# Kernel tuning notes

Hardware: AMD Instinct MI355X
Metric: run time of the kernel (lower is better)

The kernel has to match this reference:

```python
import jax, jax.numpy as jnp
import numpy as np

B, N, D, D_OUT = 8, 2048, 256, 256
LN_EPS = 1e-5
LRELU_SLOPE = 0.01


def setup_inputs() -> dict:
    key = jax.random.key(0)
    ks = jax.random.split(key, 11)
    s_in = 1.0 / np.sqrt(D)
    s_out = 1.0 / np.sqrt(D)
    return {
        "x_local": jax.random.normal(ks[0], (B, N, D), dtype=jnp.float32),
        "Wq": jax.random.uniform(ks[1], (D, D), jnp.float32, -s_in, s_in),
        "bq": jax.random.uniform(ks[2], (D,), jnp.float32, -s_in, s_in),
        "Wk": jax.random.uniform(ks[3], (D, D), jnp.float32, -s_in, s_in),
        "bk": jax.random.uniform(ks[4], (D,), jnp.float32, -s_in, s_in),
        "Wv": jax.random.uniform(ks[5], (D, D), jnp.float32, -s_in, s_in),
        "bv": jax.random.uniform(ks[6], (D,), jnp.float32, -s_in, s_in),
        "Wo": jax.random.uniform(ks[7], (D_OUT, D), jnp.float32, -s_out, s_out),
        "bo": jax.random.uniform(ks[8], (D_OUT,), jnp.float32, -s_out, s_out),
        "ln_gamma": jnp.ones((D_OUT,), jnp.float32),
        "ln_beta": jnp.zeros((D_OUT,), jnp.float32),
    }


def reference(x_local, Wq, bq, Wk, bk, Wv, bv, Wo, bo, ln_gamma, ln_beta):
    # Linear layers (torch convention: y = x @ W.T + b)
    Q = jnp.einsum("bnd,ed->bne", x_local, Wq) + bq
    K = jnp.einsum("bnd,ed->bne", x_local, Wk) + bk
    V = jnp.einsum("bnd,ed->bne", x_local, Wv) + bv
    # Unscaled attention (source applies no 1/sqrt(d))
    scores = jnp.einsum("bnd,bmd->bnm", Q, K)          # [B, N, N]
    attn = jax.nn.softmax(scores, axis=-1)
    loc = jnp.einsum("bnm,bmd->bnd", attn, V)           # [B, N, D]
    # fc_out: Linear -> LayerNorm -> LeakyReLU
    h = jnp.einsum("bnd,ed->bne", loc, Wo) + bo          # [B, N, D_OUT]
    mu = jnp.mean(h, axis=-1, keepdims=True)
    var = jnp.mean(jnp.square(h - mu), axis=-1, keepdims=True)
    hn = (h - mu) / jnp.sqrt(var + LN_EPS) * ln_gamma + ln_beta
    return jnp.where(hn >= 0, hn, LRELU_SLOPE * hn)
```

## Files before the change

### kernel.cpp

```cpp
#include <hip/hip_runtime.h>

typedef unsigned short u16;
typedef __attribute__((ext_vector_type(8))) _Float16 f16x8;
typedef __attribute__((ext_vector_type(4))) float f32x4;

#define MFMA_F16 __builtin_amdgcn_mfma_f32_16x16x32_f16

static __device__ __forceinline__ u16 f2h(float f) {
    return __builtin_bit_cast(u16, (_Float16)f);
}
static __device__ __forceinline__ ushort4 f4_to_h4(const float4 v) {
    ushort4 r;
    r.x = f2h(v.x); r.y = f2h(v.y); r.z = f2h(v.z); r.w = f2h(v.w);
    return r;
}

__global__ __launch_bounds__(256) void prep_w(
    const float* __restrict__ wq, const float* __restrict__ wk,
    const float* __restrict__ wv, const float* __restrict__ wo,
    u16* __restrict__ w4)
{
    const int tid = blockIdx.x * 256 + threadIdx.x;
    for (int i = tid; i < 65536; i += 16384) {
        const float* src = (i < 16384) ? wq : (i < 32768) ? wk
                         : (i < 49152) ? wv : wo;
        ((ushort4*)w4)[i] = f4_to_h4(((const float4*)src)[i & 16383]);
    }
}

__global__ __launch_bounds__(256) void proj_qkv(
    const float* __restrict__ X, const u16* __restrict__ w4,
    const float* __restrict__ bq, const float* __restrict__ bk,
    const float* __restrict__ bv,
    u16* __restrict__ Qh, u16* __restrict__ Kh, u16* __restrict__ Vt)
{
    const int z = blockIdx.y;
    const u16* __restrict__ W     = w4 + z * 65536;
    const float* __restrict__ bias = (z == 0) ? bq : (z == 1) ? bk : bv;

    const int m0   = blockIdx.x * 64;
    const int t    = threadIdx.x;
    const int w    = t >> 6;
    const int lane = t & 63;
    const int quad = lane >> 4;
    const int l16  = lane & 15;

    __shared__ __align__(16) u16 smem[18432];
    u16* Xs = smem;
    u16* Ws = smem + 2560;

    f32x4 acc[16];
#pragma unroll
    for (int i = 0; i < 16; ++i) acc[i] = f32x4{0.f, 0.f, 0.f, 0.f};

    for (int kc = 0; kc < 8; ++kc) {
#pragma unroll
        for (int i = 0; i < 2; ++i) {
            const int ch = i * 256 + t;
            const int row = ch >> 3, cg = ch & 7;
            const float4 v = *(const float4*)&X[(size_t)(m0 + row) * 256 + kc * 32 + cg * 4];
            *(ushort4*)&Xs[row * 40 + cg * 4] = f4_to_h4(v);
        }
#pragma unroll
        for (int i = 0; i < 4; ++i) {
            const int ch = i * 256 + t;
            const int row = ch >> 2, cg = ch & 3;
            *(int4*)&Ws[row * 40 + cg * 8] =
                *(const int4*)&W[(size_t)row * 256 + kc * 32 + cg * 8];
        }
        __syncthreads();

        const f16x8 af = *(const f16x8*)&Xs[(w * 16 + l16) * 40 + quad * 8];
#pragma unroll
        for (int nt = 0; nt < 16; ++nt) {
            const f16x8 bf = *(const f16x8*)&Ws[(nt * 16 + l16) * 40 + quad * 8];
            acc[nt] = MFMA_F16(af, bf, acc[nt], 0, 0, 0);
        }
        __syncthreads();
    }

    if (z < 2) {
        u16* __restrict__ Y = (z == 0) ? Qh : Kh;
#pragma unroll
        for (int nt = 0; nt < 16; ++nt) {
            const int col = nt * 16 + l16;
            const float bb = bias[col];
#pragma unroll
            for (int r = 0; r < 4; ++r)
                smem[(w * 16 + quad * 4 + r) * 264 + col] = f2h(acc[nt][r] + bb);
        }
        __syncthreads();
#pragma unroll
        for (int i = 0; i < 8; ++i) {
            const int ch = i * 256 + t;
            const int row = ch >> 5, cg = ch & 31;
            *(int4*)&Y[(size_t)(m0 + row) * 256 + cg * 8] =
                *(const int4*)&smem[row * 264 + cg * 8];
        }
    } else {
        const int b  = m0 >> 11;
        const int n0 = m0 & 2047;
#pragma unroll
        for (int nt = 0; nt < 16; ++nt) {
            const int col = nt * 16 + l16;
            const float bb = bias[col];
            ushort4 h4;
            h4.x = f2h(acc[nt][0] + bb);
            h4.y = f2h(acc[nt][1] + bb);
            h4.z = f2h(acc[nt][2] + bb);
            h4.w = f2h(acc[nt][3] + bb);
            *(ushort4*)&smem[col * 72 + w * 16 + quad * 4] = h4;
        }
        __syncthreads();
#pragma unroll
        for (int i = 0; i < 8; ++i) {
            const int ch = i * 256 + t;
            const int row = ch >> 3, cg = ch & 7;
            *(int4*)&Vt[(size_t)b * 524288 + (size_t)row * 2048 + n0 + cg * 8] =
                *(const int4*)&smem[row * 72 + cg * 8];
        }
    }
}

__global__ __launch_bounds__(256) void attn(
    const u16* __restrict__ Qh, const u16* __restrict__ Kg,
    const u16* __restrict__ Vt, u16* __restrict__ Op,
    u16* __restrict__ OutS, float* __restrict__ lmpL, float* __restrict__ lmpM)
{
    const int nz = gridDim.z;
    const int z  = blockIdx.z;
    const int tbase = 64 / nz, trem = 64 % nz;
    const int my_tiles = tbase + (z < trem ? 1 : 0);
    const int tile0    = tbase * z + (z < trem ? z : trem);

    const int b  = blockIdx.y;
    const int q0 = blockIdx.x * 64;
    const int t    = threadIdx.x;
    const int w    = t >> 6;
    const int lane = t & 63;
    const int quad = lane >> 4;
    const int l16  = lane & 15;

    __shared__ __align__(16) u16 smem[18688];
    u16* Ks = smem;
    u16* Vs = smem + 8448;
    u16* Os = smem;

    f16x8 qf[8];
    {
        const size_t qrow = (size_t)(b * 2048 + q0 + w * 16 + l16) * 256;
#pragma unroll
        for (int kc = 0; kc < 8; ++kc)
            qf[kc] = *(const f16x8*)&Qh[qrow + kc * 32 + quad * 8];
    }

    f32x4 O[16];
#pragma unroll
    for (int i = 0; i < 16; ++i) O[i] = f32x4{0.f, 0.f, 0.f, 0.f};
    float mrow = -1e30f, lrow = 0.f;

    for (int it = 0; it < my_tiles; ++it) {
        const int kt = (tile0 + it) * 32;
#pragma unroll
        for (int i = 0; i < 4; ++i) {
            const int ch = i * 256 + t;
            const int row = ch >> 5, cg = ch & 31;
            const int prow = ((row >> 2) & 3) * 8 + (row >> 4) * 4 + (row & 3);
            *(int4*)&Ks[row * 264 + cg * 8] =
                *(const int4*)&Kg[(size_t)(b * 2048 + kt + prow) * 256 + cg * 8];
        }
#pragma unroll
        for (int i = 0; i < 4; ++i) {
            const int ch = i * 256 + t;
            const int row = ch >> 2, cg = ch & 3;
            *(int4*)&Vs[row * 40 + cg * 8] =
                *(const int4*)&Vt[(size_t)b * 524288 + (size_t)row * 2048 + kt + cg * 8];
        }
        __syncthreads();

        f32x4 S[2];
        S[0] = f32x4{0.f, 0.f, 0.f, 0.f};
        S[1] = f32x4{0.f, 0.f, 0.f, 0.f};
        __builtin_amdgcn_s_setprio(1);
#pragma unroll
        for (int kc = 0; kc < 8; ++kc) {
#pragma unroll
            for (int kn = 0; kn < 2; ++kn) {
                const f16x8 kf = *(const f16x8*)&Ks[(kn * 16 + l16) * 264 + kc * 32 + quad * 8];
                S[kn] = MFMA_F16(kf, qf[kc], S[kn], 0, 0, 0);
            }
        }
        __builtin_amdgcn_s_setprio(0);

        float mt = fmaxf(fmaxf(fmaxf(S[0][0], S[0][1]), fmaxf(S[0][2], S[0][3])),
                         fmaxf(fmaxf(S[1][0], S[1][1]), fmaxf(S[1][2], S[1][3])));
        mt = fmaxf(mt, __shfl_xor(mt, 16));
        mt = fmaxf(mt, __shfl_xor(mt, 32));
        if (__any(mt - mrow > 8.f)) {
            const float mnew = fmaxf(mrow, mt);
            const float a = __expf(mrow - mnew);
            lrow *= a;
#pragma unroll
            for (int dv = 0; dv < 16; ++dv)
#pragma unroll
                for (int r = 0; r < 4; ++r) O[dv][r] *= a;
            mrow = mnew;
        }
        float p[2][4];
        float s = 0.f;
#pragma unroll
        for (int kn = 0; kn < 2; ++kn)
#pragma unroll
            for (int r = 0; r < 4; ++r) {
                p[kn][r] = __expf(S[kn][r] - mrow);
                s += p[kn][r];
            }
        s += __shfl_xor(s, 16);
        s += __shfl_xor(s, 32);
        lrow += s;

        f16x8 pf;
#pragma unroll
        for (int kn = 0; kn < 2; ++kn)
#pragma unroll
            for (int r = 0; r < 4; ++r)
                pf[kn * 4 + r] = (_Float16)p[kn][r];

        __builtin_amdgcn_s_setprio(1);
#pragma unroll
        for (int dvt = 0; dvt < 16; ++dvt) {
            const f16x8 vf = *(const f16x8*)&Vs[(dvt * 16 + l16) * 40 + quad * 8];
            O[dvt] = MFMA_F16(vf, pf, O[dvt], 0, 0, 0);
        }
        __builtin_amdgcn_s_setprio(0);
        __syncthreads();
    }

    {
        const float rl = 1.0f / lrow;
#pragma unroll
        for (int dvt = 0; dvt < 16; ++dvt) {
            ushort4 h4;
            h4.x = f2h(O[dvt][0] * rl);
            h4.y = f2h(O[dvt][1] * rl);
            h4.z = f2h(O[dvt][2] * rl);
            h4.w = f2h(O[dvt][3] * rl);
            *(ushort4*)&Os[(w * 16 + l16) * 264 + dvt * 16 + quad * 4] = h4;
        }
        if (quad == 0) {
            const int grow = b * 2048 + q0 + w * 16 + l16;
            lmpL[z * 16384 + grow] = lrow;
            lmpM[z * 16384 + grow] = mrow;
        }
    }
    __syncthreads();

    {
        const int row = t >> 2;
        if (z < 2) {
            u16* __restrict__ Oz = Op + (size_t)z * 4194304;
#pragma unroll
            for (int i = 0; i < 8; ++i) {
                const int chunk = (t & 3) * 8 + i;
                *(int4*)&Oz[(size_t)(b * 2048 + q0 + row) * 256 + chunk * 8] =
                    *(const int4*)&Os[row * 264 + chunk * 8];
            }
        } else {
            u16* __restrict__ Oz = OutS + (size_t)(z - 2) * 256;
#pragma unroll
            for (int i = 0; i < 8; ++i) {
                const int chunk = (t & 3) * 8 + i;
                *(int4*)&Oz[(size_t)(b * 2048 + q0 + row) * 512 + chunk * 8] =
                    *(const int4*)&Os[row * 264 + chunk * 8];
            }
        }
    }
}

__global__ __launch_bounds__(256) void outproj_ln(
    const u16* __restrict__ Op, const u16* __restrict__ OutS,
    const float* __restrict__ lmpL, const float* __restrict__ lmpM,
    const u16* __restrict__ Woh, const float* __restrict__ bo,
    const float* __restrict__ gamma, const float* __restrict__ beta,
    float* __restrict__ out)
{
    const int m0   = blockIdx.x * 64;
    const int t    = threadIdx.x;
    const int w    = t >> 6;
    const int lane = t & 63;
    const int quad = lane >> 4;
    const int l16  = lane & 15;

    __shared__ __align__(16) u16 Ls[64 * 40];
    __shared__ __align__(16) u16 Ws[256 * 40];
    __shared__ _Float16 wls[4][64];

    if (t < 64) {
        const float l0 = lmpL[m0 + t],         l1 = lmpL[16384 + m0 + t];
        const float l2 = lmpL[32768 + m0 + t], l3 = lmpL[49152 + m0 + t];
        const float m0v = lmpM[m0 + t],          m1v = lmpM[16384 + m0 + t];
        const float m2v = lmpM[32768 + m0 + t],  m3v = lmpM[49152 + m0 + t];
        const float mm = fmaxf(fmaxf(m0v, m1v), fmaxf(m2v, m3v));
        const float u0 = l0 * __expf(m0v - mm);
        const float u1 = l1 * __expf(m1v - mm);
        const float u2 = l2 * __expf(m2v - mm);
        const float u3 = l3 * __expf(m3v - mm);
        const float inv = 1.0f / (u0 + u1 + u2 + u3);
        wls[0][t] = (_Float16)(u0 * inv);
        wls[1][t] = (_Float16)(u1 * inv);
        wls[2][t] = (_Float16)(u2 * inv);
        wls[3][t] = (_Float16)(u3 * inv);
    }
    __syncthreads();

    f32x4 acc[16];
#pragma unroll
    for (int i = 0; i < 16; ++i) acc[i] = f32x4{0.f, 0.f, 0.f, 0.f};

    for (int kc = 0; kc < 8; ++kc) {
        {
            const int row = t >> 2, cg = t & 3;
            const size_t off  = (size_t)(m0 + row) * 256 + kc * 32 + cg * 8;
            const size_t offS = (size_t)(m0 + row) * 512 + kc * 32 + cg * 8;
            const f16x8 o0 = __builtin_bit_cast(f16x8, *(const int4*)&Op[off]);
            const f16x8 o1 = __builtin_bit_cast(f16x8, *(const int4*)&Op[4194304 + off]);
            const f16x8 o2 = __builtin_bit_cast(f16x8, *(const int4*)&OutS[offS]);
            const f16x8 o3 = __builtin_bit_cast(f16x8, *(const int4*)&OutS[offS + 256]);
            const _Float16 w0 = wls[0][row], w1 = wls[1][row];
            const _Float16 w2 = wls[2][row], w3 = wls[3][row];
            f16x8 lw;
#pragma unroll
            for (int j = 0; j < 8; ++j)
                lw[j] = o0[j] * w0 + o1[j] * w1 + o2[j] * w2 + o3[j] * w3;
            *(int4*)&Ls[row * 40 + cg * 8] = __builtin_bit_cast(int4, lw);
        }
#pragma unroll
        for (int i = 0; i < 4; ++i) {
            const int ch = i * 256 + t;
            const int row = ch >> 2, cg = ch & 3;
            *(int4*)&Ws[row * 40 + cg * 8] =
                *(const int4*)&Woh[(size_t)row * 256 + kc * 32 + cg * 8];
        }
        __syncthreads();

        const f16x8 af = *(const f16x8*)&Ls[(w * 16 + l16) * 40 + quad * 8];
#pragma unroll
        for (int nt = 0; nt < 16; ++nt) {
            const f16x8 bf = *(const f16x8*)&Ws[(nt * 16 + l16) * 40 + quad * 8];
            acc[nt] = MFMA_F16(af, bf, acc[nt], 0, 0, 0);
        }
        __syncthreads();
    }

    float g[16], bt[16], bb[16];
#pragma unroll
    for (int nt = 0; nt < 16; ++nt) {
        const int col = nt * 16 + l16;
        bb[nt] = bo[col]; g[nt] = gamma[col]; bt[nt] = beta[col];
    }

#pragma unroll
    for (int r = 0; r < 4; ++r) {
        float h[16];
        float sh = 0.f, sh2 = 0.f;
#pragma unroll
        for (int nt = 0; nt < 16; ++nt) {
            h[nt] = acc[nt][r] + bb[nt];
            sh  += h[nt];
            sh2 += h[nt] * h[nt];
        }
        sh  += __shfl_xor(sh, 1);  sh  += __shfl_xor(sh, 2);
        sh  += __shfl_xor(sh, 4);  sh  += __shfl_xor(sh, 8);
        sh2 += __shfl_xor(sh2, 1); sh2 += __shfl_xor(sh2, 2);
        sh2 += __shfl_xor(sh2, 4); sh2 += __shfl_xor(sh2, 8);
        const float mu  = sh * (1.f / 256.f);
        const float var = fmaxf(sh2 * (1.f / 256.f) - mu * mu, 0.f);
        const float rs  = rsqrtf(var + 1e-5f);
        const size_t row = (size_t)(m0 + w * 16 + quad * 4 + r) * 256;
#pragma unroll
        for (int nt = 0; nt < 16; ++nt) {
            const float hn = (h[nt] - mu) * rs * g[nt] + bt[nt];
            out[row + nt * 16 + l16] = (hn >= 0.f) ? hn : 0.01f * hn;
        }
    }
}

extern "C" void kernel_launch(void* const* d_in, const int* in_sizes, int n_in,
                              void* d_out, int out_size, void* d_ws, size_t ws_size,
                              hipStream_t stream)
{
    const float* x  = (const float*)d_in[0];
    const float* Wq = (const float*)d_in[1];
    const float* bq = (const float*)d_in[2];
    const float* Wk = (const float*)d_in[3];
    const float* bk = (const float*)d_in[4];
    const float* Wv = (const float*)d_in[5];
    const float* bv = (const float*)d_in[6];
    const float* Wo = (const float*)d_in[7];
    const float* bo = (const float*)d_in[8];
    const float* gm = (const float*)d_in[9];
    const float* bt = (const float*)d_in[10];
    float* out = (float*)d_out;

    u16* W4 = (u16*)d_ws;
    u16* Qh = W4 + 262144;
    u16* Kh = Qh + 4194304;
    u16* Vt = Kh + 4194304;
    u16* Op = Vt + 4194304;
    float* lmpM = (float*)(Op + 2 * 4194304);
    float* lmpL = (float*)W4;
    u16* Woh = W4 + 196608;
    u16* OutS = (u16*)d_out;

    prep_w     <<<64,             256, 0, stream>>>(Wq, Wk, Wv, Wo, W4);
    proj_qkv   <<<dim3(256, 3),   256, 0, stream>>>(x, W4, bq, bk, bv, Qh, Kh, Vt);
    attn       <<<dim3(32, 8, 4), 256, 0, stream>>>(Qh, Kh, Vt, Op, OutS, lmpL, lmpM);
    outproj_ln <<<256,            256, 0, stream>>>(Op, OutS, lmpL, lmpM, Woh, bo, gm, bt, out);
}
```

Before: 194.2 us.

## Prefetch next K-chunk into registers across projection, attention and out-proj kernels

```diff
diff --git a/kernel.cpp b/kernel.cpp
--- a/kernel.cpp
+++ b/kernel.cpp
@@ -53,28 +53,75 @@
 #pragma unroll
     for (int i = 0; i < 16; ++i) acc[i] = f32x4{0.f, 0.f, 0.f, 0.f};
 
+    float4 xst[2];
+    int4   wst[4];
+#pragma unroll
+    for (int i = 0; i < 2; ++i) {
+        const int ch = i * 256 + t;
+        const int row = ch >> 3, cg = ch & 7;
+        xst[i] = *(const float4*)&X[(size_t)(m0 + row) * 256 + cg * 4];
+    }
+#pragma unroll
+    for (int i = 0; i < 4; ++i) {
+        const int ch = i * 256 + t;
+        const int row = ch >> 2, cg = ch & 3;
+        wst[i] = *(const int4*)&W[(size_t)row * 256 + cg * 8];
+    }
+#pragma unroll
+    for (int i = 0; i < 2; ++i) {
+        const int ch = i * 256 + t;
+        const int row = ch >> 3, cg = ch & 7;
+        *(ushort4*)&Xs[row * 40 + cg * 4] = f4_to_h4(xst[i]);
+    }
+#pragma unroll
+    for (int i = 0; i < 4; ++i) {
+        const int ch = i * 256 + t;
+        const int row = ch >> 2, cg = ch & 3;
+        *(int4*)&Ws[row * 40 + cg * 8] = wst[i];
+    }
+    __syncthreads();
+
     for (int kc = 0; kc < 8; ++kc) {
-#pragma unroll
-        for (int i = 0; i < 2; ++i) {
-            const int ch = i * 256 + t;
-            const int row = ch >> 3, cg = ch & 7;
-            const float4 v = *(const float4*)&X[(size_t)(m0 + row) * 256 + kc * 32 + cg * 4];
-            *(ushort4*)&Xs[row * 40 + cg * 4] = f4_to_h4(v);
-        }
-#pragma unroll
-        for (int i = 0; i < 4; ++i) {
-            const int ch = i * 256 + t;
-            const int row = ch >> 2, cg = ch & 3;
-            *(int4*)&Ws[row * 40 + cg * 8] =
-                *(const int4*)&W[(size_t)row * 256 + kc * 32 + cg * 8];
-        }
-        __syncthreads();
+        const bool hasnext = (kc < 7);
+        if (hasnext) {
+            const int kn = kc + 1;
+#pragma unroll
+            for (int i = 0; i < 2; ++i) {
+                const int ch = i * 256 + t;
+                const int row = ch >> 3, cg = ch & 7;
+                xst[i] = *(const float4*)&X[(size_t)(m0 + row) * 256 + kn * 32 + cg * 4];
+            }
+#pragma unroll
+            for (int i = 0; i < 4; ++i) {
+                const int ch = i * 256 + t;
+                const int row = ch >> 2, cg = ch & 3;
+                wst[i] = *(const int4*)&W[(size_t)row * 256 + kn * 32 + cg * 8];
+            }
+        }
 
         const f16x8 af = *(const f16x8*)&Xs[(w * 16 + l16) * 40 + quad * 8];
+        __builtin_amdgcn_s_setprio(1);
 #pragma unroll
         for (int nt = 0; nt < 16; ++nt) {
             const f16x8 bf = *(const f16x8*)&Ws[(nt * 16 + l16) * 40 + quad * 8];
             acc[nt] = MFMA_F16(af, bf, acc[nt], 0, 0, 0);
+        }
+        __builtin_amdgcn_s_setprio(0);
+        __syncthreads();
+
+        if (hasnext) {
+#pragma unroll
+            for (int i = 0; i < 2; ++i) {
+                const int ch = i * 256 + t;
+                const int row = ch >> 3, cg = ch & 7;
+                *(ushort4*)&Xs[row * 40 + cg * 4] = f4_to_h4(xst[i]);
+            }
+#pragma unroll
+            for (int i = 0; i < 4; ++i) {
+                const int ch = i * 256 + t;
+                const int row = ch >> 2, cg = ch & 3;
+                *(int4*)&Ws[row * 40 + cg * 8] = wst[i];
+            }
         }
         __syncthreads();
     }
@@ -122,7 +169,7 @@
     }
 }
 
-__global__ __launch_bounds__(256) void attn(
+__global__ __launch_bounds__(256, 2) void attn(
     const u16* __restrict__ Qh, const u16* __restrict__ Kg,
     const u16* __restrict__ Vt, u16* __restrict__ Op,
     u16* __restrict__ OutS, float* __restrict__ lmpL, float* __restrict__ lmpM)
@@ -141,9 +188,7 @@
     const int quad = lane >> 4;
     const int l16  = lane & 15;
 
-    __shared__ __align__(16) u16 smem[18688];
-    u16* Ks = smem;
-    u16* Vs = smem + 8448;
+    __shared__ __align__(16) u16 smem[2 * 18688];
     u16* Os = smem;
 
     f16x8 qf[8];
@@ -159,24 +204,59 @@
     for (int i = 0; i < 16; ++i) O[i] = f32x4{0.f, 0.f, 0.f, 0.f};
     float mrow = -1e30f, lrow = 0.f;
 
-    for (int it = 0; it < my_tiles; ++it) {
-        const int kt = (tile0 + it) * 32;
+    int4 kst[4], vst[4];
+    {
+        const int kt = tile0 * 32;
 #pragma unroll
         for (int i = 0; i < 4; ++i) {
             const int ch = i * 256 + t;
             const int row = ch >> 5, cg = ch & 31;
             const int prow = ((row >> 2) & 3) * 8 + (row >> 4) * 4 + (row & 3);
-            *(int4*)&Ks[row * 264 + cg * 8] =
-                *(const int4*)&Kg[(size_t)(b * 2048 + kt + prow) * 256 + cg * 8];
+            kst[i] = *(const int4*)&Kg[(size_t)(b * 2048 + kt + prow) * 256 + cg * 8];
         }
 #pragma unroll
         for (int i = 0; i < 4; ++i) {
             const int ch = i * 256 + t;
             const int row = ch >> 2, cg = ch & 3;
-            *(int4*)&Vs[row * 40 + cg * 8] =
-                *(const int4*)&Vt[(size_t)b * 524288 + (size_t)row * 2048 + kt + cg * 8];
-        }
-        __syncthreads();
+            vst[i] = *(const int4*)&Vt[(size_t)b * 524288 + (size_t)row * 2048 + kt + cg * 8];
+        }
+#pragma unroll
+        for (int i = 0; i < 4; ++i) {
+            const int ch = i * 256 + t;
+            const int row = ch >> 5, cg = ch & 31;
+            *(int4*)&smem[row * 264 + cg * 8] = kst[i];
+        }
+#pragma unroll
+        for (int i = 0; i < 4; ++i) {
+            const int ch = i * 256 + t;
+            const int row = ch >> 2, cg = ch & 3;
+            *(int4*)&smem[8448 + row * 40 + cg * 8] = vst[i];
+        }
+    }
+    __syncthreads();
+
+    for (int it = 0; it < my_tiles; ++it) {
+        u16* __restrict__ Kc = smem + (it & 1) * 18688;
+        u16* __restrict__ Vc = Kc + 8448;
+        u16* __restrict__ Kn = smem + ((it & 1) ^ 1) * 18688;
+        u16* __restrict__ Vn = Kn + 8448;
+        const bool hasnext = (it + 1 < my_tiles);
+        if (hasnext) {
+            const int kt = (tile0 + it + 1) * 32;
+#pragma unroll
+            for (int i = 0; i < 4; ++i) {
+                const int ch = i * 256 + t;
+                const int row = ch >> 5, cg = ch & 31;
+                const int prow = ((row >> 2) & 3) * 8 + (row >> 4) * 4 + (row & 3);
+                kst[i] = *(const int4*)&Kg[(size_t)(b * 2048 + kt + prow) * 256 + cg * 8];
+            }
+#pragma unroll
+            for (int i = 0; i < 4; ++i) {
+                const int ch = i * 256 + t;
+                const int row = ch >> 2, cg = ch & 3;
+                vst[i] = *(const int4*)&Vt[(size_t)b * 524288 + (size_t)row * 2048 + kt + cg * 8];
+            }
+        }
 
         f32x4 S[2];
         S[0] = f32x4{0.f, 0.f, 0.f, 0.f};
@@ -186,7 +266,7 @@
         for (int kc = 0; kc < 8; ++kc) {
 #pragma unroll
             for (int kn = 0; kn < 2; ++kn) {
-                const f16x8 kf = *(const f16x8*)&Ks[(kn * 16 + l16) * 264 + kc * 32 + quad * 8];
+                const f16x8 kf = *(const f16x8*)&Kc[(kn * 16 + l16) * 264 + kc * 32 + quad * 8];
                 S[kn] = MFMA_F16(kf, qf[kc], S[kn], 0, 0, 0);
             }
         }
@@ -219,20 +299,35 @@
         s += __shfl_xor(s, 32);
         lrow += s;
 
-        f16x8 pf;
+        f16x8 pfv;
 #pragma unroll
         for (int kn = 0; kn < 2; ++kn)
 #pragma unroll
             for (int r = 0; r < 4; ++r)
-                pf[kn * 4 + r] = (_Float16)p[kn][r];
+                pfv[kn * 4 + r] = (_Float16)p[kn][r];
 
         __builtin_amdgcn_s_setprio(1);
 #pragma unroll
         for (int dvt = 0; dvt < 16; ++dvt) {
-            const f16x8 vf = *(const f16x8*)&Vs[(dvt * 16 + l16) * 40 + quad * 8];
-            O[dvt] = MFMA_F16(vf, pf, O[dvt], 0, 0, 0);
+            const f16x8 vf = *(const f16x8*)&Vc[(dvt * 16 + l16) * 40 + quad * 8];
+            O[dvt] = MFMA_F16(vf, pfv, O[dvt], 0, 0, 0);
         }
         __builtin_amdgcn_s_setprio(0);
+
+        if (hasnext) {
+#pragma unroll
+            for (int i = 0; i < 4; ++i) {
+                const int ch = i * 256 + t;
+                const int row = ch >> 5, cg = ch & 31;
+                *(int4*)&Kn[row * 264 + cg * 8] = kst[i];
+            }
+#pragma unroll
+            for (int i = 0; i < 4; ++i) {
+                const int ch = i * 256 + t;
+                const int row = ch >> 2, cg = ch & 3;
+                *(int4*)&Vn[row * 40 + cg * 8] = vst[i];
+            }
+        }
         __syncthreads();
     }
 
@@ -294,6 +389,24 @@
     __shared__ __align__(16) u16 Ls[64 * 40];
     __shared__ __align__(16) u16 Ws[256 * 40];
     __shared__ _Float16 wls[4][64];
+
+    const int orow = t >> 2, ocg = t & 3;
+
+    int4 ost[4], wst[4];
+    {
+        const size_t off  = (size_t)(m0 + orow) * 256 + ocg * 8;
+        const size_t offS = (size_t)(m0 + orow) * 512 + ocg * 8;
+        ost[0] = *(const int4*)&Op[off];
+        ost[1] = *(const int4*)&Op[4194304 + off];
+        ost[2] = *(const int4*)&OutS[offS];
+        ost[3] = *(const int4*)&OutS[offS + 256];
+    }
+#pragma unroll
+    for (int i = 0; i < 4; ++i) {
+        const int ch = i * 256 + t;
+        const int row = ch >> 2, cg = ch & 3;
+        wst[i] = *(const int4*)&Woh[(size_t)row * 256 + cg * 8];
+    }
 
     if (t < 64) {
         const float l0 = lmpL[m0 + t],         l1 = lmpL[16384 + m0 + t];
@@ -313,41 +426,77 @@
     }
     __syncthreads();
 
+    {
+        const _Float16 w0 = wls[0][orow], w1 = wls[1][orow];
+        const _Float16 w2 = wls[2][orow], w3 = wls[3][orow];
+        const f16x8 o0 = __builtin_bit_cast(f16x8, ost[0]);
+        const f16x8 o1 = __builtin_bit_cast(f16x8, ost[1]);
+        const f16x8 o2 = __builtin_bit_cast(f16x8, ost[2]);
+        const f16x8 o3 = __builtin_bit_cast(f16x8, ost[3]);
+        f16x8 lw;
+#pragma unroll
+        for (int j = 0; j < 8; ++j)
+            lw[j] = o0[j] * w0 + o1[j] * w1 + o2[j] * w2 + o3[j] * w3;
+        *(int4*)&Ls[orow * 40 + ocg * 8] = __builtin_bit_cast(int4, lw);
+    }
+#pragma unroll
+    for (int i = 0; i < 4; ++i) {
+        const int ch = i * 256 + t;
+        const int row = ch >> 2, cg = ch & 3;
+        *(int4*)&Ws[row * 40 + cg * 8] = wst[i];
+    }
+    __syncthreads();
+
     f32x4 acc[16];
 #pragma unroll
     for (int i = 0; i < 16; ++i) acc[i] = f32x4{0.f, 0.f, 0.f, 0.f};
 
     for (int kc = 0; kc < 8; ++kc) {
-        {
-            const int row = t >> 2, cg = t & 3;
-            const size_t off  = (size_t)(m0 + row) * 256 + kc * 32 + cg * 8;
-            const size_t offS = (size_t)(m0 + row) * 512 + kc * 32 + cg * 8;
-            const f16x8 o0 = __builtin_bit_cast(f16x8, *(const int4*)&Op[off]);
-            const f16x8 o1 = __builtin_bit_cast(f16x8, *(const int4*)&Op[4194304 + off]);
-            const f16x8 o2 = __builtin_bit_cast(f16x8, *(const int4*)&OutS[offS]);
-            const f16x8 o3 = __builtin_bit_cast(f16x8, *(const int4*)&OutS[offS + 256]);
-            const _Float16 w0 = wls[0][row], w1 = wls[1][row];
-            const _Float16 w2 = wls[2][row], w3 = wls[3][row];
-            f16x8 lw;
-#pragma unroll
-            for (int j = 0; j < 8; ++j)
-                lw[j] = o0[j] * w0 + o1[j] * w1 + o2[j] * w2 + o3[j] * w3;
-            *(int4*)&Ls[row * 40 + cg * 8] = __builtin_bit_cast(int4, lw);
-        }
-#pragma unroll
-        for (int i = 0; i < 4; ++i) {
-            const int ch = i * 256 + t;
-            const int row = ch >> 2, cg = ch & 3;
-            *(int4*)&Ws[row * 40 + cg * 8] =
-                *(const int4*)&Woh[(size_t)row * 256 + kc * 32 + cg * 8];
-        }
-        __syncthreads();
+        const bool hasnext = (kc < 7);
+        if (hasnext) {
+            const int kn = kc + 1;
+            const size_t off  = (size_t)(m0 + orow) * 256 + kn * 32 + ocg * 8;
+            const size_t offS = (size_t)(m0 + orow) * 512 + kn * 32 + ocg * 8;
+            ost[0] = *(const int4*)&Op[off];
+            ost[1] = *(const int4*)&Op[4194304 + off];
+            ost[2] = *(const int4*)&OutS[offS];
+            ost[3] = *(const int4*)&OutS[offS + 256];
+#pragma unroll
+            for (int i = 0; i < 4; ++i) {
+                const int ch = i * 256 + t;
+                const int row = ch >> 2, cg = ch & 3;
+                wst[i] = *(const int4*)&Woh[(size_t)row * 256 + kn * 32 + cg * 8];
+            }
+        }
 
         const f16x8 af = *(const f16x8*)&Ls[(w * 16 + l16) * 40 + quad * 8];
+        __builtin_amdgcn_s_setprio(1);
 #pragma unroll
         for (int nt = 0; nt < 16; ++nt) {
             const f16x8 bf = *(const f16x8*)&Ws[(nt * 16 + l16) * 40 + quad * 8];
             acc[nt] = MFMA_F16(af, bf, acc[nt], 0, 0, 0);
+        }
+        __builtin_amdgcn_s_setprio(0);
+        __syncthreads();
+
+        if (hasnext) {
+            const _Float16 w0 = wls[0][orow], w1 = wls[1][orow];
+            const _Float16 w2 = wls[2][orow], w3 = wls[3][orow];
+            const f16x8 o0 = __builtin_bit_cast(f16x8, ost[0]);
+            const f16x8 o1 = __builtin_bit_cast(f16x8, ost[1]);
+            const f16x8 o2 = __builtin_bit_cast(f16x8, ost[2]);
+            const f16x8 o3 = __builtin_bit_cast(f16x8, ost[3]);
+            f16x8 lw;
+#pragma unroll
+            for (int j = 0; j < 8; ++j)
+                lw[j] = o0[j] * w0 + o1[j] * w1 + o2[j] * w2 + o3[j] * w3;
+            *(int4*)&Ls[orow * 40 + ocg * 8] = __builtin_bit_cast(int4, lw);
+#pragma unroll
+            for (int i = 0; i < 4; ++i) {
+                const int ch = i * 256 + t;
+                const int row = ch >> 2, cg = ch & 3;
+                *(int4*)&Ws[row * 40 + cg * 8] = wst[i];
+            }
         }
         __syncthreads();
     }
```

Result: slower. 306.6 us (+57.9%).

## Use three-way key split in attention with occupancy hint and fused P conversion

Applied to the files above, without the earlier changes.

```diff
diff --git a/kernel.cpp b/kernel.cpp
--- a/kernel.cpp
+++ b/kernel.cpp
@@ -122,7 +122,7 @@
     }
 }
 
-__global__ __launch_bounds__(256) void attn(
+__global__ __launch_bounds__(256, 3) void attn(
     const u16* __restrict__ Qh, const u16* __restrict__ Kg,
     const u16* __restrict__ Vt, u16* __restrict__ Op,
     u16* __restrict__ OutS, float* __restrict__ lmpL, float* __restrict__ lmpM)
@@ -206,31 +206,25 @@
                 for (int r = 0; r < 4; ++r) O[dv][r] *= a;
             mrow = mnew;
         }
-        float p[2][4];
+        f16x8 pfv;
         float s = 0.f;
 #pragma unroll
         for (int kn = 0; kn < 2; ++kn)
 #pragma unroll
             for (int r = 0; r < 4; ++r) {
-                p[kn][r] = __expf(S[kn][r] - mrow);
-                s += p[kn][r];
+                const float e = __expf(S[kn][r] - mrow);
+                s += e;
+                pfv[kn * 4 + r] = (_Float16)e;
             }
         s += __shfl_xor(s, 16);
         s += __shfl_xor(s, 32);
         lrow += s;
 
-        f16x8 pf;
-#pragma unroll
-        for (int kn = 0; kn < 2; ++kn)
-#pragma unroll
-            for (int r = 0; r < 4; ++r)
-                pf[kn * 4 + r] = (_Float16)p[kn][r];
-
         __builtin_amdgcn_s_setprio(1);
 #pragma unroll
         for (int dvt = 0; dvt < 16; ++dvt) {
             const f16x8 vf = *(const f16x8*)&Vs[(dvt * 16 + l16) * 40 + quad * 8];
-            O[dvt] = MFMA_F16(vf, pf, O[dvt], 0, 0, 0);
+            O[dvt] = MFMA_F16(vf, pfv, O[dvt], 0, 0, 0);
         }
         __builtin_amdgcn_s_setprio(0);
         __syncthreads();
@@ -266,7 +260,7 @@
                     *(const int4*)&Os[row * 264 + chunk * 8];
             }
         } else {
-            u16* __restrict__ Oz = OutS + (size_t)(z - 2) * 256;
+            u16* __restrict__ Oz = OutS;
 #pragma unroll
             for (int i = 0; i < 8; ++i) {
                 const int chunk = (t & 3) * 8 + i;
@@ -293,23 +287,23 @@
 
     __shared__ __align__(16) u16 Ls[64 * 40];
     __shared__ __align__(16) u16 Ws[256 * 40];
-    __shared__ _Float16 wls[4][64];
+    __shared__ _Float16 wls[3][64];
 
     if (t < 64) {
-        const float l0 = lmpL[m0 + t],         l1 = lmpL[16384 + m0 + t];
-        const float l2 = lmpL[32768 + m0 + t], l3 = lmpL[49152 + m0 + t];
-        const float m0v = lmpM[m0 + t],          m1v = lmpM[16384 + m0 + t];
-        const float m2v = lmpM[32768 + m0 + t],  m3v = lmpM[49152 + m0 + t];
-        const float mm = fmaxf(fmaxf(m0v, m1v), fmaxf(m2v, m3v));
+        const float l0 = lmpL[m0 + t];
+        const float l1 = lmpL[16384 + m0 + t];
+        const float l2 = lmpL[32768 + m0 + t];
+        const float m0v = lmpM[m0 + t];
+        const float m1v = lmpM[16384 + m0 + t];
+        const float m2v = lmpM[32768 + m0 + t];
+        const float mm = fmaxf(fmaxf(m0v, m1v), m2v);
         const float u0 = l0 * __expf(m0v - mm);
         const float u1 = l1 * __expf(m1v - mm);
         const float u2 = l2 * __expf(m2v - mm);
-        const float u3 = l3 * __expf(m3v - mm);
-        const float inv = 1.0f / (u0 + u1 + u2 + u3);
+        const float inv = 1.0f / (u0 + u1 + u2);
         wls[0][t] = (_Float16)(u0 * inv);
         wls[1][t] = (_Float16)(u1 * inv);
         wls[2][t] = (_Float16)(u2 * inv);
-        wls[3][t] = (_Float16)(u3 * inv);
     }
     __syncthreads();
 
@@ -325,13 +319,11 @@
             const f16x8 o0 = __builtin_bit_cast(f16x8, *(const int4*)&Op[off]);
             const f16x8 o1 = __builtin_bit_cast(f16x8, *(const int4*)&Op[4194304 + off]);
             const f16x8 o2 = __builtin_bit_cast(f16x8, *(const int4*)&OutS[offS]);
-            const f16x8 o3 = __builtin_bit_cast(f16x8, *(const int4*)&OutS[offS + 256]);
-            const _Float16 w0 = wls[0][row], w1 = wls[1][row];
-            const _Float16 w2 = wls[2][row], w3 = wls[3][row];
+            const _Float16 w0 = wls[0][row], w1 = wls[1][row], w2 = wls[2][row];
             f16x8 lw;
 #pragma unroll
             for (int j = 0; j < 8; ++j)
-                lw[j] = o0[j] * w0 + o1[j] * w1 + o2[j] * w2 + o3[j] * w3;
+                lw[j] = o0[j] * w0 + o1[j] * w1 + o2[j] * w2;
             *(int4*)&Ls[row * 40 + cg * 8] = __builtin_bit_cast(int4, lw);
         }
 #pragma unroll
@@ -414,6 +406,6 @@
 
     prep_w     <<<64,             256, 0, stream>>>(Wq, Wk, Wv, Wo, W4);
     proj_qkv   <<<dim3(256, 3),   256, 0, stream>>>(x, W4, bq, bk, bv, Qh, Kh, Vt);
-    attn       <<<dim3(32, 8, 4), 256, 0, stream>>>(Qh, Kh, Vt, Op, OutS, lmpL, lmpM);
+    attn       <<<dim3(32, 8, 3), 256, 0, stream>>>(Qh, Kh, Vt, Op, OutS, lmpL, lmpM);
     outproj_ln <<<256,            256, 0, stream>>>(Op, OutS, lmpL, lmpM, Woh, bo, gm, bt, out);
 }
```

Result: faster. 181.2 us (-6.7%).
